# Kernel optimization log

Measured on AMD Instinct MI355X. Metric: run time of the kernel, lower is better.

The kernel has to match this reference:

```python
import jax, jax.numpy as jnp
import numpy as np

COS_EPS = 1e-8      # torch F.cosine_similarity default eps
NORM_EPS = 1e-16    # renormalization eps in address()


def setup_inputs() -> dict:
    B, N, M = 64, 16384, 64
    key = jax.random.key(0)
    ks = jax.random.split(key, 7)
    key_vector = jax.random.normal(ks[0], (B, M), dtype=jnp.float32)
    key_strength = jax.random.uniform(ks[1], (B, 1), dtype=jnp.float32) * 5.0
    gate = jax.random.uniform(ks[2], (B, 1), dtype=jnp.float32)
    shift_raw = jax.random.uniform(ks[3], (B, 3), dtype=jnp.float32)
    shift = shift_raw / jnp.sum(shift_raw, axis=1, keepdims=True)  # softmax-like shift dist
    sharpen = 1.0 + jax.random.uniform(ks[4], (B, 1), dtype=jnp.float32)  # >= 1 as in NTM
    la_raw = jax.random.uniform(ks[5], (B, N), dtype=jnp.float32)
    last_address = la_raw / jnp.sum(la_raw, axis=1, keepdims=True)  # valid weighting
    memory = jax.random.normal(ks[6], (B, N, M), dtype=jnp.float32) * 0.1
    return {
        "key_vector": key_vector,
        "key_strength": key_strength,
        "gate": gate,
        "shift": shift,
        "sharpen": sharpen,
        "last_address": last_address,
        "memory": memory,
    }


def reference(key_vector, key_strength, gate, shift, sharpen, last_address, memory):
    # --- content addressing: cosine similarity of key vs every memory row ---
    dot = jnp.einsum("bm,bnm->bn", key_vector, memory)            # [B, N]
    k_norm = jnp.linalg.norm(key_vector, axis=-1, keepdims=True)  # [B, 1]
    m_norm = jnp.linalg.norm(memory, axis=-1)                     # [B, N]
    cos = dot / jnp.maximum(k_norm * m_norm, COS_EPS)
    wc = jax.nn.softmax(key_strength * cos, axis=1)               # [B, N]
    # --- interpolation gate ---
    wg = gate * wc + (1.0 - gate) * last_address                  # [B, N]
    # --- circular convolution with size-3 shift kernel ---
    # torch conv1d is cross-correlation: ws[j] = s0*w[j-1] + s1*w[j] + s2*w[j+1] (circular)
    ws = (shift[:, 0:1] * jnp.roll(wg, 1, axis=1)
          + shift[:, 1:2] * wg
          + shift[:, 2:3] * jnp.roll(wg, -1, axis=1))             # [B, N]
    # --- sharpening + renormalization ---
    ws = ws ** sharpen
    wt = ws / (jnp.sum(ws, axis=1, keepdims=True) + NORM_EPS)
    return wt
```

## Files before the change

### kernel.cpp

```cpp
#include <hip/hip_runtime.h>
#include <math.h>

#define B_ 64
#define N_ 16384
#define M_ 64

__global__ __launch_bounds__(256) void scores_kernel(
    const float* __restrict__ key, const float* __restrict__ beta,
    const float* __restrict__ memory, float* __restrict__ s_out)
{
    const int b    = blockIdx.y;
    const int tid  = threadIdx.x;
    const int lane = tid & 63;
    const int wave = tid >> 6;
    const int l    = lane & 15;
    const int g    = lane >> 4;

    const float4 k4 = *reinterpret_cast<const float4*>(key + b * M_ + l * 4);
    float ksq = k4.x * k4.x + k4.y * k4.y + k4.z * k4.z + k4.w * k4.w;
#pragma unroll
    for (int m = 1; m < 16; m <<= 1) ksq += __shfl_xor(ksq, m);
    const float knorm = sqrtf(ksq);
    const float kb    = beta[b];

    const float* __restrict__ mb = memory + (size_t)b * N_ * M_;
    float* __restrict__ sb       = s_out + (size_t)b * N_;

    const int rowBase = blockIdx.x * 256 + wave * 64;
#pragma unroll 4
    for (int i = 0; i < 16; ++i) {
        const int r = rowBase + i * 4 + g;
        const float4 m4 = *reinterpret_cast<const float4*>(mb + (size_t)r * M_ + l * 4);
        float dot = k4.x * m4.x + k4.y * m4.y + k4.z * m4.z + k4.w * m4.w;
        float msq = m4.x * m4.x + m4.y * m4.y + m4.z * m4.z + m4.w * m4.w;
#pragma unroll
        for (int m = 1; m < 16; m <<= 1) {
            dot += __shfl_xor(dot, m);
            msq += __shfl_xor(msq, m);
        }
        if (l == 0) {
            const float denom = fmaxf(knorm * sqrtf(msq), 1e-8f);
            sb[r] = kb * dot / denom;
        }
    }
}

__global__ __launch_bounds__(1024) void addr_kernel(
    const float* __restrict__ gate, const float* __restrict__ shift,
    const float* __restrict__ sharpen, const float* __restrict__ la,
    float* __restrict__ out)
{
    const int b    = blockIdx.x;
    const int t    = threadIdx.x;
    const int lane = t & 63;
    const int wv   = t >> 6;

    __shared__ float red[16];
    __shared__ float lft[1024];
    __shared__ float rgt[1024];

    float* __restrict__ ob        = out + (size_t)b * N_;
    const float* __restrict__ lab = la + (size_t)b * N_;

    float s[16];
#pragma unroll
    for (int q = 0; q < 4; ++q)
        *reinterpret_cast<float4*>(&s[4 * q]) =
            reinterpret_cast<const float4*>(ob)[t * 4 + q];

    float mx = s[0];
#pragma unroll
    for (int i = 1; i < 16; ++i) mx = fmaxf(mx, s[i]);
#pragma unroll
    for (int m = 1; m < 64; m <<= 1) mx = fmaxf(mx, __shfl_xor(mx, m));
    if (lane == 0) red[wv] = mx;
    __syncthreads();
    mx = red[0];
#pragma unroll
    for (int i = 1; i < 16; ++i) mx = fmaxf(mx, red[i]);
    __syncthreads();

    float zs = 0.f;
#pragma unroll
    for (int i = 0; i < 16; ++i) { s[i] = expf(s[i] - mx); zs += s[i]; }
#pragma unroll
    for (int m = 1; m < 64; m <<= 1) zs += __shfl_xor(zs, m);
    if (lane == 0) red[wv] = zs;
    __syncthreads();
    float Z = red[0];
#pragma unroll
    for (int i = 1; i < 16; ++i) Z += red[i];
    __syncthreads();
    const float invZ = 1.0f / Z;

    const float gg = gate[b];
    const float om = 1.0f - gg;
    float wl[16];
#pragma unroll
    for (int q = 0; q < 4; ++q)
        *reinterpret_cast<float4*>(&wl[4 * q]) =
            reinterpret_cast<const float4*>(lab)[t * 4 + q];
    float wg[16];
#pragma unroll
    for (int i = 0; i < 16; ++i) wg[i] = gg * (s[i] * invZ) + om * wl[i];

    lft[t] = wg[0];
    rgt[t] = wg[15];
    __syncthreads();
    const float prev = rgt[(t + 1023) & 1023];
    const float nxt  = lft[(t + 1) & 1023];
    const float s0 = shift[b * 3 + 0];
    const float s1 = shift[b * 3 + 1];
    const float s2 = shift[b * 3 + 2];
    float ws[16];
    ws[0] = s0 * prev + s1 * wg[0] + s2 * wg[1];
#pragma unroll
    for (int i = 1; i < 15; ++i) ws[i] = s0 * wg[i - 1] + s1 * wg[i] + s2 * wg[i + 1];
    ws[15] = s0 * wg[14] + s1 * wg[15] + s2 * nxt;

    const float p = sharpen[b];
    float ssum = 0.f;
#pragma unroll
    for (int i = 0; i < 16; ++i) { ws[i] = powf(ws[i], p); ssum += ws[i]; }
#pragma unroll
    for (int m = 1; m < 64; m <<= 1) ssum += __shfl_xor(ssum, m);
    __syncthreads();
    if (lane == 0) red[wv] = ssum;
    __syncthreads();
    float S = red[0];
#pragma unroll
    for (int i = 1; i < 16; ++i) S += red[i];
    const float inv = 1.0f / (S + 1e-16f);

#pragma unroll
    for (int q = 0; q < 4; ++q) {
        float4 o;
        o.x = ws[4 * q + 0] * inv;
        o.y = ws[4 * q + 1] * inv;
        o.z = ws[4 * q + 2] * inv;
        o.w = ws[4 * q + 3] * inv;
        reinterpret_cast<float4*>(ob)[t * 4 + q] = o;
    }
}

extern "C" void kernel_launch(void* const* d_in, const int* in_sizes, int n_in,
                              void* d_out, int out_size, void* d_ws, size_t ws_size,
                              hipStream_t stream) {
    const float* key     = (const float*)d_in[0];
    const float* beta    = (const float*)d_in[1];
    const float* gate    = (const float*)d_in[2];
    const float* shift   = (const float*)d_in[3];
    const float* sharpen = (const float*)d_in[4];
    const float* la      = (const float*)d_in[5];
    const float* memory  = (const float*)d_in[6];
    float* out = (float*)d_out;

    dim3 gridA(N_ / 256, B_);
    scores_kernel<<<gridA, 256, 0, stream>>>(key, beta, memory, out);

    addr_kernel<<<B_, 1024, 0, stream>>>(gate, shift, sharpen, la, out);
}
```

Baseline: 396.8 us.

## Remap lanes to 4 per row, fuse exp into scores, drop softmax max pass

```diff
diff --git a/kernel.cpp b/kernel.cpp
--- a/kernel.cpp
+++ b/kernel.cpp
@@ -4,6 +4,8 @@
 #define B_ 64
 #define N_ 16384
 #define M_ 64
+
+typedef float vfloat4 __attribute__((ext_vector_type(4)));
 
 __global__ __launch_bounds__(256) void scores_kernel(
     const float* __restrict__ key, const float* __restrict__ beta,
@@ -13,13 +15,20 @@
     const int tid  = threadIdx.x;
     const int lane = tid & 63;
     const int wave = tid >> 6;
-    const int l    = lane & 15;
-    const int g    = lane >> 4;
+    const int l    = lane & 3;
+    const int rr   = lane >> 2;
 
-    const float4 k4 = *reinterpret_cast<const float4*>(key + b * M_ + l * 4);
-    float ksq = k4.x * k4.x + k4.y * k4.y + k4.z * k4.z + k4.w * k4.w;
+    vfloat4 k4[4];
 #pragma unroll
-    for (int m = 1; m < 16; m <<= 1) ksq += __shfl_xor(ksq, m);
+    for (int j = 0; j < 4; ++j)
+        k4[j] = *reinterpret_cast<const vfloat4*>(key + b * M_ + j * 16 + l * 4);
+
+    float ksq = 0.f;
+#pragma unroll
+    for (int j = 0; j < 4; ++j)
+        ksq += k4[j].x * k4[j].x + k4[j].y * k4[j].y + k4[j].z * k4[j].z + k4[j].w * k4[j].w;
+    ksq += __shfl_xor(ksq, 1);
+    ksq += __shfl_xor(ksq, 2);
     const float knorm = sqrtf(ksq);
     const float kb    = beta[b];
 
@@ -27,20 +36,28 @@
     float* __restrict__ sb       = s_out + (size_t)b * N_;
 
     const int rowBase = blockIdx.x * 256 + wave * 64;
-#pragma unroll 4
-    for (int i = 0; i < 16; ++i) {
-        const int r = rowBase + i * 4 + g;
-        const float4 m4 = *reinterpret_cast<const float4*>(mb + (size_t)r * M_ + l * 4);
-        float dot = k4.x * m4.x + k4.y * m4.y + k4.z * m4.z + k4.w * m4.w;
-        float msq = m4.x * m4.x + m4.y * m4.y + m4.z * m4.z + m4.w * m4.w;
 #pragma unroll
-        for (int m = 1; m < 16; m <<= 1) {
-            dot += __shfl_xor(dot, m);
-            msq += __shfl_xor(msq, m);
+    for (int t = 0; t < 4; ++t) {
+        const int row = rowBase + t * 16 + rr;
+        const float* rp = mb + (size_t)row * M_;
+        vfloat4 m4[4];
+#pragma unroll
+        for (int j = 0; j < 4; ++j)
+            m4[j] = __builtin_nontemporal_load(
+                reinterpret_cast<const vfloat4*>(rp + j * 16 + l * 4));
+
+        float dot = 0.f, msq = 0.f;
+#pragma unroll
+        for (int j = 0; j < 4; ++j) {
+            dot += k4[j].x * m4[j].x + k4[j].y * m4[j].y + k4[j].z * m4[j].z + k4[j].w * m4[j].w;
+            msq += m4[j].x * m4[j].x + m4[j].y * m4[j].y + m4[j].z * m4[j].z + m4[j].w * m4[j].w;
         }
+        dot += __shfl_xor(dot, 1);  dot += __shfl_xor(dot, 2);
+        msq += __shfl_xor(msq, 1);  msq += __shfl_xor(msq, 2);
+
         if (l == 0) {
             const float denom = fmaxf(knorm * sqrtf(msq), 1e-8f);
-            sb[r] = kb * dot / denom;
+            sb[row] = expf(kb * dot / denom);
         }
     }
 }
@@ -68,21 +85,9 @@
         *reinterpret_cast<float4*>(&s[4 * q]) =
             reinterpret_cast<const float4*>(ob)[t * 4 + q];
 
-    float mx = s[0];
-#pragma unroll
-    for (int i = 1; i < 16; ++i) mx = fmaxf(mx, s[i]);
-#pragma unroll
-    for (int m = 1; m < 64; m <<= 1) mx = fmaxf(mx, __shfl_xor(mx, m));
-    if (lane == 0) red[wv] = mx;
-    __syncthreads();
-    mx = red[0];
-#pragma unroll
-    for (int i = 1; i < 16; ++i) mx = fmaxf(mx, red[i]);
-    __syncthreads();
-
     float zs = 0.f;
 #pragma unroll
-    for (int i = 0; i < 16; ++i) { s[i] = expf(s[i] - mx); zs += s[i]; }
+    for (int i = 0; i < 16; ++i) zs += s[i];
 #pragma unroll
     for (int m = 1; m < 64; m <<= 1) zs += __shfl_xor(zs, m);
     if (lane == 0) red[wv] = zs;
@@ -121,7 +126,7 @@
     const float p = sharpen[b];
     float ssum = 0.f;
 #pragma unroll
-    for (int i = 0; i < 16; ++i) { ws[i] = powf(ws[i], p); ssum += ws[i]; }
+    for (int i = 0; i < 16; ++i) { ws[i] = exp2f(p * log2f(ws[i])); ssum += ws[i]; }
 #pragma unroll
     for (int m = 1; m < 64; m <<= 1) ssum += __shfl_xor(ssum, m);
     __syncthreads();
```

Measured after the change: 357.4 us. -9.9%, faster.
